# Performance work log

Measured on AMD Instinct MI355X. Metric: run time of the kernel, lower is better.

## Reference

```python
import jax, jax.numpy as jnp
import numpy as np

NG = 100000   # number of g-side nodes
NS = 100000   # number of s-side nodes
E = 640000    # edges per direction
D = 128       # feature / embed dim


def setup_inputs() -> dict:
    key = jax.random.key(0)
    ks = jax.random.split(key, 16)
    inp = {
        'Xg_self':  jax.random.normal(ks[0], (NG, D), jnp.float32),
        'Xs_self':  jax.random.normal(ks[1], (NS, D), jnp.float32),
        'Xs_for_g': jax.random.normal(ks[2], (NS, D), jnp.float32),
        'Xg_for_s': jax.random.normal(ks[3], (NG, D), jnp.float32),
        # COO edge lists for the two bipartite sparse adjacencies
        'row_gs': jax.random.randint(ks[4], (E,), 0, NG, jnp.int32),
        'col_gs': jax.random.randint(ks[5], (E,), 0, NS, jnp.int32),
        'val_gs': jax.random.uniform(ks[6], (E,), jnp.float32),
        'row_sg': jax.random.randint(ks[7], (E,), 0, NS, jnp.int32),
        'col_sg': jax.random.randint(ks[8], (E,), 0, NG, jnp.int32),
        'val_sg': jax.random.uniform(ks[9], (E,), jnp.float32),
        # Linear weights (PyTorch layout: [out_features, in_features], no bias)
        'Wg_self':  jax.random.normal(ks[10], (D, D), jnp.float32) * 0.05,
        'Wg_neigh': jax.random.normal(ks[11], (D, D), jnp.float32) * 0.05,
        'Ws_self':  jax.random.normal(ks[12], (D, D), jnp.float32) * 0.05,
        'Ws_neigh': jax.random.normal(ks[13], (D, D), jnp.float32) * 0.05,
    }
    return inp


def reference(Xg_self, Xs_self, Xs_for_g, Xg_for_s,
              row_gs, col_gs, val_gs, row_sg, col_sg, val_sg,
              Wg_self, Wg_neigh, Ws_self, Ws_neigh):
    # SpMM: neigh_g = A_gs @ Xs_for_g  (Ng x Ns sparse times Ns x D dense)
    neigh_g = jax.ops.segment_sum(Xs_for_g[col_gs] * val_gs[:, None], row_gs,
                                  num_segments=NG)
    # SpMM: neigh_s = A_sg @ Xg_for_s
    neigh_s = jax.ops.segment_sum(Xg_for_s[col_sg] * val_sg[:, None], row_sg,
                                  num_segments=NS)
    out_g = jax.nn.relu(Xg_self @ Wg_self.T + neigh_g @ Wg_neigh.T)
    out_s = jax.nn.relu(Xs_self @ Ws_self.T + neigh_s @ Ws_neigh.T)
    return (out_g, out_s)
```

## Files before the change

### kernel.cpp

```cpp
#include <hip/hip_runtime.h>
#include <hip/hip_bf16.h>
#include <stdint.h>

typedef __attribute__((ext_vector_type(4))) float f32x4;
typedef __attribute__((ext_vector_type(8))) short bf16x8;

#define D 128
#define GLOBAL_AS __attribute__((address_space(1)))
#define LDS_AS __attribute__((address_space(3)))

__device__ inline short f2bf(float x) {
    __hip_bfloat16 h = __float2bfloat16(x);
    return __builtin_bit_cast(short, h);
}

__device__ inline bf16x8 pack8(f32x4 lo, f32x4 hi) {
    bf16x8 b;
    b[0] = f2bf(lo[0]); b[1] = f2bf(lo[1]); b[2] = f2bf(lo[2]); b[3] = f2bf(lo[3]);
    b[4] = f2bf(hi[0]); b[5] = f2bf(hi[1]); b[6] = f2bf(hi[2]); b[7] = f2bf(hi[3]);
    return b;
}

__device__ inline unsigned int pack2bf(float a, float b) {
    unsigned int ua = (unsigned int)(unsigned short)f2bf(a);
    unsigned int ub = (unsigned int)(unsigned short)f2bf(b);
    return ua | (ub << 16);
}


__global__ __launch_bounds__(256)
void prep_kernel(const float* __restrict__ Xa, const float* __restrict__ Xb,
                 unsigned short* __restrict__ x16a, unsigned short* __restrict__ x16b,
                 const float* __restrict__ Wg_self, const float* __restrict__ Wg_neigh,
                 const float* __restrict__ Ws_self, const float* __restrict__ Ws_neigh,
                 short* __restrict__ Wcat,
                 const int* __restrict__ rowA, int EA,
                 const int* __restrict__ rowB, int NGoff,
                 int* __restrict__ cnt,
                 int n8a, int n8b, int Etot)
{
    int t = blockIdx.x * 256 + threadIdx.x;
    if (t < n8a) {
        f32x4 lo = *reinterpret_cast<const f32x4*>(Xa + (size_t)t * 8);
        f32x4 hi = *reinterpret_cast<const f32x4*>(Xa + (size_t)t * 8 + 4);
        *reinterpret_cast<bf16x8*>(x16a + (size_t)t * 8) = pack8(lo, hi);
        return;
    }
    t -= n8a;
    if (t < n8b) {
        f32x4 lo = *reinterpret_cast<const f32x4*>(Xb + (size_t)t * 8);
        f32x4 hi = *reinterpret_cast<const f32x4*>(Xb + (size_t)t * 8 + 4);
        *reinterpret_cast<bf16x8*>(x16b + (size_t)t * 8) = pack8(lo, hi);
        return;
    }
    t -= n8b;
    if (t < 2 * 128 * 32) {
        int dir = t >> 12;
        int rem = t & 4095;
        int j = rem >> 5;
        int k = (rem & 31) * 8;
        const float* Wself  = dir ? Ws_self  : Wg_self;
        const float* Wneigh = dir ? Ws_neigh : Wg_neigh;
        const float* src = (k < 128) ? (Wself + j * D + k) : (Wneigh + j * D + (k - 128));
        f32x4 lo = *reinterpret_cast<const f32x4*>(src);
        f32x4 hi = *reinterpret_cast<const f32x4*>(src + 4);
        *reinterpret_cast<bf16x8*>(Wcat + (size_t)dir * 32768 + j * 256 + k) = pack8(lo, hi);
        return;
    }
    t -= 2 * 128 * 32;
    if (t < Etot) {
        int r = (t < EA) ? rowA[t] : (rowB[t - EA] + NGoff);
        atomicAdd(&cnt[r], 1);
    }
}


__global__ __launch_bounds__(256)
void scan1_kernel(const int* __restrict__ cnt, int* __restrict__ part,
                  int* __restrict__ blksums, int N)
{
    __shared__ int wsum[4];
    int t = threadIdx.x;
    int base = blockIdx.x * 1024 + t * 4;
    int v0 = base + 0 < N ? cnt[base + 0] : 0;
    int v1 = base + 1 < N ? cnt[base + 1] : 0;
    int v2 = base + 2 < N ? cnt[base + 2] : 0;
    int v3 = base + 3 < N ? cnt[base + 3] : 0;
    int s = v0 + v1 + v2 + v3;
    int lane = t & 63, w = t >> 6;
    int x = s;
#pragma unroll
    for (int off = 1; off < 64; off <<= 1) {
        int y = __shfl_up(x, off);
        if (lane >= off) x += y;
    }
    if (lane == 63) wsum[w] = x;
    __syncthreads();
    int woff = 0;
    for (int i = 0; i < w; ++i) woff += wsum[i];
    int incl = x + woff;
    int excl = incl - s;
    if (base + 0 < N) part[base + 0] = excl;
    if (base + 1 < N) part[base + 1] = excl + v0;
    if (base + 2 < N) part[base + 2] = excl + v0 + v1;
    if (base + 3 < N) part[base + 3] = excl + v0 + v1 + v2;
    if (t == 255) blksums[blockIdx.x] = incl;
}

__global__ __launch_bounds__(256)
void scan2_kernel(int* __restrict__ blksums, int nb)
{
    __shared__ int wsum[4];
    int t = threadIdx.x;
    int v = t < nb ? blksums[t] : 0;
    int lane = t & 63, w = t >> 6;
    int x = v;
#pragma unroll
    for (int off = 1; off < 64; off <<= 1) {
        int y = __shfl_up(x, off);
        if (lane >= off) x += y;
    }
    if (lane == 63) wsum[w] = x;
    __syncthreads();
    int woff = 0;
    for (int i = 0; i < w; ++i) woff += wsum[i];
    int excl = x + woff - v;
    if (t < nb) blksums[t] = excl;
}

__global__ __launch_bounds__(256)
void scan3_kernel(int* __restrict__ cursor, const int* __restrict__ blksums, int N)
{
    int i = blockIdx.x * 256 + threadIdx.x;
    if (i < N) cursor[i] += blksums[i >> 10];
}

__global__ __launch_bounds__(256)
void fill2_kernel(const int* __restrict__ rowA, const int* __restrict__ colA,
                  const float* __restrict__ valA, int EA,
                  const int* __restrict__ rowB, const int* __restrict__ colB,
                  const float* __restrict__ valB, int NGoff,
                  int* __restrict__ cursor, int2* __restrict__ pairs, int Etot)
{
    int e = blockIdx.x * 256 + threadIdx.x;
    if (e >= Etot) return;
    int r, c; float v;
    if (e < EA) { r = rowA[e]; c = colA[e]; v = valA[e]; }
    else { int e2 = e - EA; r = rowB[e2] + NGoff; c = colB[e2]; v = valB[e2]; }
    int p = atomicAdd(&cursor[r], 1);
    pairs[p] = make_int2(c, __float_as_int(v));
}

__global__ __launch_bounds__(512, 6)
void fused_kernel(const unsigned short* __restrict__ X16_0,
                  const unsigned short* __restrict__ X16_1,
                  const float* __restrict__ Xself0, float* __restrict__ out0, int n0,
                  const float* __restrict__ Xself1, float* __restrict__ out1, int n1,
                  const int* __restrict__ cnt, const int* __restrict__ endpos,
                  const int2* __restrict__ pairs, const short* __restrict__ Wcat)
{
    __shared__ float  As[32 * 128];
    __shared__ bf16x8 Ab[32 * 16];

    const int ROWS = 32;
    int blocks0 = (n0 + ROWS - 1) / ROWS;

    const unsigned short* X16; const float* Xself; float* out;
    int nRows, r0base, csr0; const short* Wb;
    if ((int)blockIdx.x < blocks0) {
        X16 = X16_0; Xself = Xself0; out = out0; nRows = n0;
        r0base = blockIdx.x * ROWS; csr0 = 0; Wb = Wcat;
    } else {
        X16 = X16_1; Xself = Xself1; out = out1; nRows = n1;
        r0base = ((int)blockIdx.x - blocks0) * ROWS; csr0 = n0; Wb = Wcat + 32768;
    }

    const int tid  = threadIdx.x;
    const int wave = tid >> 6, lane = tid & 63;
    const int l15  = lane & 15, lhi = lane >> 4;
    const int l31  = lane & 31;
    const int hw   = tid >> 5;

#pragma unroll
    for (int q = 0; q < 2; ++q) {
        int rs = wave * 4 + q * 2 + (lane >> 5);
        int R = r0base + rs; if (R > nRows - 1) R = nRows - 1;
        const float* g = Xself + (size_t)R * D + (((lane & 31) ^ (rs & 7)) << 2);
        __builtin_amdgcn_global_load_lds((const GLOBAL_AS uint32_t*)g,
                                         (LDS_AS uint32_t*)(&As[(wave * 4 + q * 2) * 128]),
                                         16, 0, 0);
    }

    uint2* Ab64 = (uint2*)Ab;
#pragma unroll 1
    for (int ii = 0; ii < 2; ++ii) {
        int r = hw * 2 + ii;
        int R = r0base + r; if (R > nRows - 1) R = nRows - 1;
        int gid = csr0 + R;
        int n = cnt[gid];
        int s = endpos[gid] - n;
        f32x4 acc = {0.f, 0.f, 0.f, 0.f};
#pragma unroll 1
        for (int j = 0; j < n; j += 8) {
            int2 p[8]; uint2 xb[8];
#pragma unroll
            for (int u = 0; u < 8; ++u) {
                int idx = (j + u < n) ? j + u : n - 1;
                p[u] = pairs[s + idx];
            }
#pragma unroll
            for (int u = 0; u < 8; ++u)
                xb[u] = *reinterpret_cast<const uint2*>(X16 + (size_t)p[u].x * D + l31 * 4);
#pragma unroll
            for (int u = 0; u < 8; ++u) {
                float v = (j + u < n) ? __int_as_float(p[u].y) : 0.f;
                acc[0] += __uint_as_float(xb[u].x << 16) * v;
                acc[1] += __uint_as_float(xb[u].x & 0xffff0000u) * v;
                acc[2] += __uint_as_float(xb[u].y << 16) * v;
                acc[3] += __uint_as_float(xb[u].y & 0xffff0000u) * v;
            }
        }
        uint2 nb = { pack2bf(acc[0], acc[1]), pack2bf(acc[2], acc[3]) };
        int cn = (l31 >> 1) ^ (r & 7);
        Ab64[r * 32 + cn * 2 + (l31 & 1)] = nb;
    }

    bf16x8 bfrag[8];
    {
        int j = wave * 16 + l15;
#pragma unroll
        for (int kb = 0; kb < 8; ++kb)
            bfrag[kb] = *reinterpret_cast<const bf16x8*>(
                Wb + (size_t)j * 256 + kb * 32 + lhi * 8);
    }

    __syncthreads();

#pragma unroll
    for (int it = 0; it < 2; ++it) {
        int r = it * 16 + l15;
        int rx = r & 7;
        f32x4 acc = {0.f, 0.f, 0.f, 0.f};
#pragma unroll
        for (int kb = 0; kb < 8; ++kb) {
            bf16x8 af;
            if (kb < 4) {
                int c0 = kb * 8 + lhi * 2;
                f32x4 lo = *reinterpret_cast<const f32x4*>(&As[r * 128 + ((c0 ^ rx) << 2)]);
                f32x4 hi = *reinterpret_cast<const f32x4*>(&As[r * 128 + (((c0 + 1) ^ rx) << 2)]);
                af = pack8(lo, hi);
            } else {
                int cn = (kb - 4) * 4 + lhi;
                af = Ab[r * 16 + (cn ^ rx)];
            }
            acc = __builtin_amdgcn_mfma_f32_16x16x32_bf16(af, bfrag[kb], acc, 0, 0, 0);
        }
#pragma unroll
        for (int i2 = 0; i2 < 4; ++i2) {
            int rr = r0base + it * 16 + lhi * 4 + i2;
            if (rr < nRows) {
                float v = acc[i2] > 0.f ? acc[i2] : 0.f;
                out[(size_t)rr * D + wave * 16 + l15] = v;
            }
        }
    }
}


__global__ __launch_bounds__(256)
void scatter_edges(const float* __restrict__ X, const int* __restrict__ row,
                   const int* __restrict__ col, const float* __restrict__ val,
                   float* out, int nE)
{
    int t = blockIdx.x * 256 + threadIdx.x;
    int e = t >> 5;
    if (e >= nE) return;
    int l = t & 31;
    int r = row[e];
    int c = col[e];
    float v = val[e];
    f32x4 x = *reinterpret_cast<const f32x4*>(X + (size_t)c * D + l * 4);
    float* o = out + (size_t)r * D + l * 4;
    unsafeAtomicAdd(o + 0, x[0] * v);
    unsafeAtomicAdd(o + 1, x[1] * v);
    unsafeAtomicAdd(o + 2, x[2] * v);
    unsafeAtomicAdd(o + 3, x[3] * v);
}

__global__ __launch_bounds__(256)
void gemm_relu_fb(const float* __restrict__ Xself, const float* __restrict__ Neigh,
                  const float* __restrict__ Wself, const float* __restrict__ Wneigh,
                  float* __restrict__ out, int nRows)
{
    const int tid  = threadIdx.x;
    const int wave = tid >> 6;
    const int lane = tid & 63;
    const int l15  = lane & 15;
    const int lhi  = lane >> 4;

    bf16x8 bfrag[2][8];
#pragma unroll
    for (int n = 0; n < 2; ++n) {
        int j = wave * 32 + n * 16 + l15;
#pragma unroll
        for (int kb = 0; kb < 8; ++kb) {
            int k = kb * 32 + lhi * 8;
            const float* src = (kb < 4) ? (Wself + j * D + k)
                                        : (Wneigh + j * D + (k - 128));
            f32x4 lo = *reinterpret_cast<const f32x4*>(src);
            f32x4 hi = *reinterpret_cast<const f32x4*>(src + 4);
            bfrag[n][kb] = pack8(lo, hi);
        }
    }

    int r0base = blockIdx.x * 128;
#pragma unroll 1
    for (int it = 0; it < 8; ++it) {
        int r0 = r0base + it * 16;
        if (r0 >= nRows) break;
        const float* xrow = Xself + (size_t)(r0 + l15) * D;
        const float* nrow = Neigh + (size_t)(r0 + l15) * D;
        bf16x8 afrag[8];
#pragma unroll
        for (int kb = 0; kb < 8; ++kb) {
            const float* src = (kb < 4) ? (xrow + kb * 32 + lhi * 8)
                                        : (nrow + (kb - 4) * 32 + lhi * 8);
            f32x4 lo = *reinterpret_cast<const f32x4*>(src);
            f32x4 hi = *reinterpret_cast<const f32x4*>(src + 4);
            afrag[kb] = pack8(lo, hi);
        }
        asm volatile("s_waitcnt vmcnt(0)" ::: "memory");
        __syncthreads();

        f32x4 acc0 = {0.f, 0.f, 0.f, 0.f};
        f32x4 acc1 = {0.f, 0.f, 0.f, 0.f};
#pragma unroll
        for (int kb = 0; kb < 8; ++kb) {
            acc0 = __builtin_amdgcn_mfma_f32_16x16x32_bf16(afrag[kb], bfrag[0][kb], acc0, 0, 0, 0);
            acc1 = __builtin_amdgcn_mfma_f32_16x16x32_bf16(afrag[kb], bfrag[1][kb], acc1, 0, 0, 0);
        }
#pragma unroll
        for (int i = 0; i < 4; ++i) {
            int rr = r0 + lhi * 4 + i;
            if (rr < nRows) {
                float v0 = acc0[i] > 0.f ? acc0[i] : 0.f;
                float v1 = acc1[i] > 0.f ? acc1[i] : 0.f;
                out[(size_t)rr * D + wave * 32 + l15]      = v0;
                out[(size_t)rr * D + wave * 32 + 16 + l15] = v1;
            }
        }
    }
}


extern "C" void kernel_launch(void* const* d_in, const int* in_sizes, int n_in,
                              void* d_out, int out_size, void* d_ws, size_t ws_size,
                              hipStream_t stream)
{
    const float* Xg_self  = (const float*)d_in[0];
    const float* Xs_self  = (const float*)d_in[1];
    const float* Xs_for_g = (const float*)d_in[2];
    const float* Xg_for_s = (const float*)d_in[3];
    const int*   row_gs   = (const int*)d_in[4];
    const int*   col_gs   = (const int*)d_in[5];
    const float* val_gs   = (const float*)d_in[6];
    const int*   row_sg   = (const int*)d_in[7];
    const int*   col_sg   = (const int*)d_in[8];
    const float* val_sg   = (const float*)d_in[9];
    const float* Wg_self  = (const float*)d_in[10];
    const float* Wg_neigh = (const float*)d_in[11];
    const float* Ws_self  = (const float*)d_in[12];
    const float* Ws_neigh = (const float*)d_in[13];

    const int NG = in_sizes[0] / D;
    const int NS = in_sizes[1] / D;
    const int E1 = in_sizes[4];
    const int E2 = in_sizes[7];
    const int N  = NG + NS;
    const int Etot = E1 + E2;

    float* out_g = (float*)d_out;
    float* out_s = out_g + (size_t)NG * D;

    size_t off = 0;
    auto alloc = [&](size_t bytes) -> size_t {
        off = (off + 255) & ~(size_t)255;
        size_t o = off;
        off += bytes;
        return o;
    };
    size_t x16g_o   = alloc(sizeof(short) * (size_t)NG * D);
    size_t x16s_o   = alloc(sizeof(short) * (size_t)NS * D);
    size_t wcat_o   = alloc(sizeof(short) * 2 * 128 * 256);
    size_t cnt_o    = alloc(sizeof(int) * N);
    size_t cursor_o = alloc(sizeof(int) * N);
    size_t pairs_o  = alloc(sizeof(int2) * (size_t)Etot);
    size_t blk_o    = alloc(sizeof(int) * 1024);
    size_t need_bytes = off;

    char* ws = (char*)d_ws;

    if (ws_size < need_bytes) {
        hipMemsetAsync(d_out, 0, (size_t)out_size * sizeof(float), stream);
        {
            long long threads = (long long)E1 * 32;
            scatter_edges<<<(int)((threads + 255) / 256), 256, 0, stream>>>(
                Xs_for_g, row_gs, col_gs, val_gs, out_g, E1);
        }
        {
            long long threads = (long long)E2 * 32;
            scatter_edges<<<(int)((threads + 255) / 256), 256, 0, stream>>>(
                Xg_for_s, row_sg, col_sg, val_sg, out_s, E2);
        }
        gemm_relu_fb<<<(NG + 127) / 128, 256, 0, stream>>>(Xg_self, out_g, Wg_self, Wg_neigh, out_g, NG);
        gemm_relu_fb<<<(NS + 127) / 128, 256, 0, stream>>>(Xs_self, out_s, Ws_self, Ws_neigh, out_s, NS);
        return;
    }

    unsigned short* x16g = (unsigned short*)(ws + x16g_o);
    unsigned short* x16s = (unsigned short*)(ws + x16s_o);
    short* wcat  = (short*)(ws + wcat_o);
    int* cnt     = (int*)(ws + cnt_o);
    int* cursor  = (int*)(ws + cursor_o);
    int2* pairs  = (int2*)(ws + pairs_o);
    int* blk     = (int*)(ws + blk_o);

    const int n8a = NG * D / 8, n8b = NS * D / 8;

    hipMemsetAsync(cnt, 0, sizeof(int) * N, stream);

    {
        long long tot = (long long)n8a + n8b + 2 * 128 * 32 + Etot;
        prep_kernel<<<(int)((tot + 255) / 256), 256, 0, stream>>>(
            Xs_for_g, Xg_for_s, x16g, x16s,
            Wg_self, Wg_neigh, Ws_self, Ws_neigh, wcat,
            row_gs, E1, row_sg, NG, cnt, n8a, n8b, Etot);
    }

    int nb = (N + 1023) / 1024;
    scan1_kernel<<<nb, 256, 0, stream>>>(cnt, cursor, blk, N);
    scan2_kernel<<<1, 256, 0, stream>>>(blk, nb);
    scan3_kernel<<<(N + 255) / 256, 256, 0, stream>>>(cursor, blk, N);
    fill2_kernel<<<(Etot + 255) / 256, 256, 0, stream>>>(
        row_gs, col_gs, val_gs, E1, row_sg, col_sg, val_sg, NG, cursor, pairs, Etot);

    int blocks0 = (NG + 31) / 32, blocks1 = (NS + 31) / 32;
    fused_kernel<<<blocks0 + blocks1, 512, 0, stream>>>(
        x16g, x16s,
        Xg_self, out_g, NG,
        Xs_self, out_s, NS,
        cnt, cursor, pairs, wcat);
}
```

Before: 297.6 us.

## Gather fp32 features directly and widen fused kernel to 1024 threads

Drops the pre-pass that converted both neighbor feature matrices to bf16, so the SpMM gather now reads fp32 rows straight from the inputs. The fused kernel grows to 1024 threads with one row per half-wave and a 2x8 wave grid of MFMA tiles. The self features are loaded and packed to bf16 per lane into a single shared A tile, replacing the async global-to-LDS copy. This removes roughly 100 MB of conversion traffic, but doubles the bytes moved per gathered edge and lowers unroll depth, which may reduce memory-level parallelism.

```diff
diff --git a/kernel.cpp b/kernel.cpp
--- a/kernel.cpp
+++ b/kernel.cpp
@@ -6,8 +6,6 @@
 typedef __attribute__((ext_vector_type(8))) short bf16x8;
 
 #define D 128
-#define GLOBAL_AS __attribute__((address_space(1)))
-#define LDS_AS __attribute__((address_space(3)))
 
 __device__ inline short f2bf(float x) {
     __hip_bfloat16 h = __float2bfloat16(x);
@@ -29,31 +27,14 @@
 
 
 __global__ __launch_bounds__(256)
-void prep_kernel(const float* __restrict__ Xa, const float* __restrict__ Xb,
-                 unsigned short* __restrict__ x16a, unsigned short* __restrict__ x16b,
-                 const float* __restrict__ Wg_self, const float* __restrict__ Wg_neigh,
+void prep_kernel(const float* __restrict__ Wg_self, const float* __restrict__ Wg_neigh,
                  const float* __restrict__ Ws_self, const float* __restrict__ Ws_neigh,
                  short* __restrict__ Wcat,
                  const int* __restrict__ rowA, int EA,
                  const int* __restrict__ rowB, int NGoff,
-                 int* __restrict__ cnt,
-                 int n8a, int n8b, int Etot)
+                 int* __restrict__ cnt, int Etot)
 {
     int t = blockIdx.x * 256 + threadIdx.x;
-    if (t < n8a) {
-        f32x4 lo = *reinterpret_cast<const f32x4*>(Xa + (size_t)t * 8);
-        f32x4 hi = *reinterpret_cast<const f32x4*>(Xa + (size_t)t * 8 + 4);
-        *reinterpret_cast<bf16x8*>(x16a + (size_t)t * 8) = pack8(lo, hi);
-        return;
-    }
-    t -= n8a;
-    if (t < n8b) {
-        f32x4 lo = *reinterpret_cast<const f32x4*>(Xb + (size_t)t * 8);
-        f32x4 hi = *reinterpret_cast<const f32x4*>(Xb + (size_t)t * 8 + 4);
-        *reinterpret_cast<bf16x8*>(x16b + (size_t)t * 8) = pack8(lo, hi);
-        return;
-    }
-    t -= n8b;
     if (t < 2 * 128 * 32) {
         int dir = t >> 12;
         int rem = t & 4095;
@@ -151,27 +132,25 @@
     pairs[p] = make_int2(c, __float_as_int(v));
 }
 
-__global__ __launch_bounds__(512, 6)
-void fused_kernel(const unsigned short* __restrict__ X16_0,
-                  const unsigned short* __restrict__ X16_1,
+__global__ __launch_bounds__(1024, 8)
+void fused_kernel(const float* __restrict__ X0, const float* __restrict__ X1,
                   const float* __restrict__ Xself0, float* __restrict__ out0, int n0,
                   const float* __restrict__ Xself1, float* __restrict__ out1, int n1,
                   const int* __restrict__ cnt, const int* __restrict__ endpos,
                   const int2* __restrict__ pairs, const short* __restrict__ Wcat)
 {
-    __shared__ float  As[32 * 128];
-    __shared__ bf16x8 Ab[32 * 16];
+    __shared__ bf16x8 A[32 * 32];
 
     const int ROWS = 32;
     int blocks0 = (n0 + ROWS - 1) / ROWS;
 
-    const unsigned short* X16; const float* Xself; float* out;
+    const float *X, *Xself; float* out;
     int nRows, r0base, csr0; const short* Wb;
     if ((int)blockIdx.x < blocks0) {
-        X16 = X16_0; Xself = Xself0; out = out0; nRows = n0;
+        X = X0; Xself = Xself0; out = out0; nRows = n0;
         r0base = blockIdx.x * ROWS; csr0 = 0; Wb = Wcat;
     } else {
-        X16 = X16_1; Xself = Xself1; out = out1; nRows = n1;
+        X = X1; Xself = Xself1; out = out1; nRows = n1;
         r0base = ((int)blockIdx.x - blocks0) * ROWS; csr0 = n0; Wb = Wcat + 32768;
     }
 
@@ -181,53 +160,48 @@
     const int l31  = lane & 31;
     const int hw   = tid >> 5;
 
-#pragma unroll
-    for (int q = 0; q < 2; ++q) {
-        int rs = wave * 4 + q * 2 + (lane >> 5);
-        int R = r0base + rs; if (R > nRows - 1) R = nRows - 1;
-        const float* g = Xself + (size_t)R * D + (((lane & 31) ^ (rs & 7)) << 2);
-        __builtin_amdgcn_global_load_lds((const GLOBAL_AS uint32_t*)g,
-                                         (LDS_AS uint32_t*)(&As[(wave * 4 + q * 2) * 128]),
-                                         16, 0, 0);
-    }
-
-    uint2* Ab64 = (uint2*)Ab;
-#pragma unroll 1
-    for (int ii = 0; ii < 2; ++ii) {
-        int r = hw * 2 + ii;
+    {
+        int r = hw;
         int R = r0base + r; if (R > nRows - 1) R = nRows - 1;
         int gid = csr0 + R;
         int n = cnt[gid];
         int s = endpos[gid] - n;
         f32x4 acc = {0.f, 0.f, 0.f, 0.f};
 #pragma unroll 1
-        for (int j = 0; j < n; j += 8) {
-            int2 p[8]; uint2 xb[8];
-#pragma unroll
-            for (int u = 0; u < 8; ++u) {
+        for (int j = 0; j < n; j += 4) {
+            int2 p[4]; f32x4 xb[4];
+#pragma unroll
+            for (int u = 0; u < 4; ++u) {
                 int idx = (j + u < n) ? j + u : n - 1;
                 p[u] = pairs[s + idx];
             }
 #pragma unroll
-            for (int u = 0; u < 8; ++u)
-                xb[u] = *reinterpret_cast<const uint2*>(X16 + (size_t)p[u].x * D + l31 * 4);
-#pragma unroll
-            for (int u = 0; u < 8; ++u) {
+            for (int u = 0; u < 4; ++u)
+                xb[u] = *reinterpret_cast<const f32x4*>(X + (size_t)p[u].x * D + l31 * 4);
+#pragma unroll
+            for (int u = 0; u < 4; ++u) {
                 float v = (j + u < n) ? __int_as_float(p[u].y) : 0.f;
-                acc[0] += __uint_as_float(xb[u].x << 16) * v;
-                acc[1] += __uint_as_float(xb[u].x & 0xffff0000u) * v;
-                acc[2] += __uint_as_float(xb[u].y << 16) * v;
-                acc[3] += __uint_as_float(xb[u].y & 0xffff0000u) * v;
+                acc[0] += xb[u][0] * v;
+                acc[1] += xb[u][1] * v;
+                acc[2] += xb[u][2] * v;
+                acc[3] += xb[u][3] * v;
             }
         }
-        uint2 nb = { pack2bf(acc[0], acc[1]), pack2bf(acc[2], acc[3]) };
-        int cn = (l31 >> 1) ^ (r & 7);
-        Ab64[r * 32 + cn * 2 + (l31 & 1)] = nb;
+        f32x4 xs = *reinterpret_cast<const f32x4*>(Xself + (size_t)R * D + l31 * 4);
+        uint2 sb  = { pack2bf(xs[0],  xs[1]),  pack2bf(xs[2],  xs[3])  };
+        uint2 nbv = { pack2bf(acc[0], acc[1]), pack2bf(acc[2], acc[3]) };
+        int rx = r & 7;
+        int eS = (l31 >> 1) ^ rx;
+        int eN = 16 + ((l31 >> 1) ^ rx);
+        uint2* A64 = (uint2*)A;
+        A64[(r * 32 + eS) * 2 + (l31 & 1)] = sb;
+        A64[(r * 32 + eN) * 2 + (l31 & 1)] = nbv;
     }
 
     bf16x8 bfrag[8];
     {
-        int j = wave * 16 + l15;
+        int ct = wave & 7;
+        int j = ct * 16 + l15;
 #pragma unroll
         for (int kb = 0; kb < 8; ++kb)
             bfrag[kb] = *reinterpret_cast<const bf16x8*>(
@@ -236,31 +210,23 @@
 
     __syncthreads();
 
-#pragma unroll
-    for (int it = 0; it < 2; ++it) {
-        int r = it * 16 + l15;
+    {
+        int rt = wave >> 3, ct = wave & 7;
+        int r = rt * 16 + l15;
         int rx = r & 7;
         f32x4 acc = {0.f, 0.f, 0.f, 0.f};
 #pragma unroll
         for (int kb = 0; kb < 8; ++kb) {
-            bf16x8 af;
-            if (kb < 4) {
-                int c0 = kb * 8 + lhi * 2;
-                f32x4 lo = *reinterpret_cast<const f32x4*>(&As[r * 128 + ((c0 ^ rx) << 2)]);
-                f32x4 hi = *reinterpret_cast<const f32x4*>(&As[r * 128 + (((c0 + 1) ^ rx) << 2)]);
-                af = pack8(lo, hi);
-            } else {
-                int cn = (kb - 4) * 4 + lhi;
-                af = Ab[r * 16 + (cn ^ rx)];
-            }
+            int e = kb * 4 + lhi;
+            bf16x8 af = A[r * 32 + (e ^ rx)];
             acc = __builtin_amdgcn_mfma_f32_16x16x32_bf16(af, bfrag[kb], acc, 0, 0, 0);
         }
 #pragma unroll
-        for (int i2 = 0; i2 < 4; ++i2) {
-            int rr = r0base + it * 16 + lhi * 4 + i2;
+        for (int i = 0; i < 4; ++i) {
+            int rr = r0base + rt * 16 + lhi * 4 + i;
             if (rr < nRows) {
-                float v = acc[i2] > 0.f ? acc[i2] : 0.f;
-                out[(size_t)rr * D + wave * 16 + l15] = v;
+                float v = acc[i] > 0.f ? acc[i] : 0.f;
+                out[(size_t)rr * D + ct * 16 + l15] = v;
             }
         }
     }
@@ -389,8 +355,6 @@
         off += bytes;
         return o;
     };
-    size_t x16g_o   = alloc(sizeof(short) * (size_t)NG * D);
-    size_t x16s_o   = alloc(sizeof(short) * (size_t)NS * D);
     size_t wcat_o   = alloc(sizeof(short) * 2 * 128 * 256);
     size_t cnt_o    = alloc(sizeof(int) * N);
     size_t cursor_o = alloc(sizeof(int) * N);
@@ -417,24 +381,19 @@
         return;
     }
 
-    unsigned short* x16g = (unsigned short*)(ws + x16g_o);
-    unsigned short* x16s = (unsigned short*)(ws + x16s_o);
     short* wcat  = (short*)(ws + wcat_o);
     int* cnt     = (int*)(ws + cnt_o);
     int* cursor  = (int*)(ws + cursor_o);
     int2* pairs  = (int2*)(ws + pairs_o);
     int* blk     = (int*)(ws + blk_o);
 
-    const int n8a = NG * D / 8, n8b = NS * D / 8;
-
     hipMemsetAsync(cnt, 0, sizeof(int) * N, stream);
 
     {
-        long long tot = (long long)n8a + n8b + 2 * 128 * 32 + Etot;
+        long long tot = (long long)2 * 128 * 32 + Etot;
         prep_kernel<<<(int)((tot + 255) / 256), 256, 0, stream>>>(
-            Xs_for_g, Xg_for_s, x16g, x16s,
             Wg_self, Wg_neigh, Ws_self, Ws_neigh, wcat,
-            row_gs, E1, row_sg, NG, cnt, n8a, n8b, Etot);
+            row_gs, E1, row_sg, NG, cnt, Etot);
     }
 
     int nb = (N + 1023) / 1024;
@@ -445,8 +404,8 @@
         row_gs, col_gs, val_gs, E1, row_sg, col_sg, val_sg, NG, cursor, pairs, Etot);
 
     int blocks0 = (NG + 31) / 32, blocks1 = (NS + 31) / 32;
-    fused_kernel<<<blocks0 + blocks1, 512, 0, stream>>>(
-        x16g, x16s,
+    fused_kernel<<<blocks0 + blocks1, 1024, 0, stream>>>(
+        Xs_for_g, Xg_for_s,
         Xg_self, out_g, NG,
         Xs_self, out_s, NS,
         cnt, cursor, pairs, wcat);
```

Result: slower. 328.8 us (+10.5%).

## Shrink fused SAGE tile to 16 rows with unified bf16 LDS operand

Applied to the files above, without the earlier changes.

The fused gather+GEMM kernel now handles 16 rows per 512-thread block instead of 32. Each half-wave gathers one row's neighbours and also loads its self features directly, converting both to bf16 into a single swizzled LDS tile. This replaces the async global-to-LDS fp32 staging and the in-loop fp32-to-bf16 packing. It also lowers LDS use and raises the occupancy hint from 6 to 8, giving more blocks and more parallel gather latency hiding. In exchange, each block reloads the same weight fragments for half as many rows, and the self-feature load now runs serially after the gather loop.

```diff
diff --git a/kernel.cpp b/kernel.cpp
--- a/kernel.cpp
+++ b/kernel.cpp
@@ -6,8 +6,6 @@
 typedef __attribute__((ext_vector_type(8))) short bf16x8;
 
 #define D 128
-#define GLOBAL_AS __attribute__((address_space(1)))
-#define LDS_AS __attribute__((address_space(3)))
 
 __device__ inline short f2bf(float x) {
     __hip_bfloat16 h = __float2bfloat16(x);
@@ -151,7 +149,7 @@
     pairs[p] = make_int2(c, __float_as_int(v));
 }
 
-__global__ __launch_bounds__(512, 6)
+__global__ __launch_bounds__(512, 8)
 void fused_kernel(const unsigned short* __restrict__ X16_0,
                   const unsigned short* __restrict__ X16_1,
                   const float* __restrict__ Xself0, float* __restrict__ out0, int n0,
@@ -159,10 +157,9 @@
                   const int* __restrict__ cnt, const int* __restrict__ endpos,
                   const int2* __restrict__ pairs, const short* __restrict__ Wcat)
 {
-    __shared__ float  As[32 * 128];
-    __shared__ bf16x8 Ab[32 * 16];
-
-    const int ROWS = 32;
+    __shared__ bf16x8 A[16 * 32];
+
+    const int ROWS = 16;
     int blocks0 = (n0 + ROWS - 1) / ROWS;
 
     const unsigned short* X16; const float* Xself; float* out;
@@ -181,20 +178,8 @@
     const int l31  = lane & 31;
     const int hw   = tid >> 5;
 
-#pragma unroll
-    for (int q = 0; q < 2; ++q) {
-        int rs = wave * 4 + q * 2 + (lane >> 5);
-        int R = r0base + rs; if (R > nRows - 1) R = nRows - 1;
-        const float* g = Xself + (size_t)R * D + (((lane & 31) ^ (rs & 7)) << 2);
-        __builtin_amdgcn_global_load_lds((const GLOBAL_AS uint32_t*)g,
-                                         (LDS_AS uint32_t*)(&As[(wave * 4 + q * 2) * 128]),
-                                         16, 0, 0);
-    }
-
-    uint2* Ab64 = (uint2*)Ab;
-#pragma unroll 1
-    for (int ii = 0; ii < 2; ++ii) {
-        int r = hw * 2 + ii;
+    {
+        int r = hw;
         int R = r0base + r; if (R > nRows - 1) R = nRows - 1;
         int gid = csr0 + R;
         int n = cnt[gid];
@@ -220,9 +205,15 @@
                 acc[3] += __uint_as_float(xb[u].y & 0xffff0000u) * v;
             }
         }
-        uint2 nb = { pack2bf(acc[0], acc[1]), pack2bf(acc[2], acc[3]) };
-        int cn = (l31 >> 1) ^ (r & 7);
-        Ab64[r * 32 + cn * 2 + (l31 & 1)] = nb;
+        f32x4 xs = *reinterpret_cast<const f32x4*>(Xself + (size_t)R * D + l31 * 4);
+        uint2 sb  = { pack2bf(xs[0],  xs[1]),  pack2bf(xs[2],  xs[3])  };
+        uint2 nbv = { pack2bf(acc[0], acc[1]), pack2bf(acc[2], acc[3]) };
+        int rx = r & 7;
+        int eS = (l31 >> 1) ^ rx;
+        int eN = 16 + ((l31 >> 1) ^ rx);
+        uint2* A64 = (uint2*)A;
+        A64[(r * 32 + eS) * 2 + (l31 & 1)] = sb;
+        A64[(r * 32 + eN) * 2 + (l31 & 1)] = nbv;
     }
 
     bf16x8 bfrag[8];
@@ -236,30 +227,21 @@
 
     __syncthreads();
 
-#pragma unroll
-    for (int it = 0; it < 2; ++it) {
-        int r = it * 16 + l15;
+    {
+        int r = l15;
         int rx = r & 7;
         f32x4 acc = {0.f, 0.f, 0.f, 0.f};
 #pragma unroll
         for (int kb = 0; kb < 8; ++kb) {
-            bf16x8 af;
-            if (kb < 4) {
-                int c0 = kb * 8 + lhi * 2;
-                f32x4 lo = *reinterpret_cast<const f32x4*>(&As[r * 128 + ((c0 ^ rx) << 2)]);
-                f32x4 hi = *reinterpret_cast<const f32x4*>(&As[r * 128 + (((c0 + 1) ^ rx) << 2)]);
-                af = pack8(lo, hi);
-            } else {
-                int cn = (kb - 4) * 4 + lhi;
-                af = Ab[r * 16 + (cn ^ rx)];
-            }
+            int e = kb * 4 + lhi;
+            bf16x8 af = A[r * 32 + (e ^ rx)];
             acc = __builtin_amdgcn_mfma_f32_16x16x32_bf16(af, bfrag[kb], acc, 0, 0, 0);
         }
 #pragma unroll
-        for (int i2 = 0; i2 < 4; ++i2) {
-            int rr = r0base + it * 16 + lhi * 4 + i2;
+        for (int i = 0; i < 4; ++i) {
+            int rr = r0base + lhi * 4 + i;
             if (rr < nRows) {
-                float v = acc[i2] > 0.f ? acc[i2] : 0.f;
+                float v = acc[i] > 0.f ? acc[i] : 0.f;
                 out[(size_t)rr * D + wave * 16 + l15] = v;
             }
         }
@@ -444,7 +426,7 @@
     fill2_kernel<<<(Etot + 255) / 256, 256, 0, stream>>>(
         row_gs, col_gs, val_gs, E1, row_sg, col_sg, val_sg, NG, cursor, pairs, Etot);
 
-    int blocks0 = (NG + 31) / 32, blocks1 = (NS + 31) / 32;
+    int blocks0 = (NG + 15) / 16, blocks1 = (NS + 15) / 16;
     fused_kernel<<<blocks0 + blocks1, 512, 0, stream>>>(
         x16g, x16s,
         Xg_self, out_g, NG,
```

Result: slower. 350.0 us (+17.6%).

## Split fused gather+GEMM into separate gather and GEMM kernels via bf16 buffer

Applied to the files above, without the earlier changes.

Un-fuses the neighbour aggregation from the GEMM. A new gather kernel uses one wave per row with 64 lanes reading 2 bf16 each and writes the aggregated neighbours to a bf16 workspace buffer. A separate 256-thread GEMM kernel loads those rows straight into MFMA fragments, with each wave computing two 16-column tiles. The aim is to decouple the latency-bound irregular gather from the MFMA stage and improve occupancy for each, at the cost of an extra kernel launch and a write and read of an N×128 bf16 intermediate.

```diff
diff --git a/kernel.cpp b/kernel.cpp
--- a/kernel.cpp
+++ b/kernel.cpp
@@ -151,116 +151,125 @@
     pairs[p] = make_int2(c, __float_as_int(v));
 }
 
-__global__ __launch_bounds__(512, 6)
-void fused_kernel(const unsigned short* __restrict__ X16_0,
-                  const unsigned short* __restrict__ X16_1,
-                  const float* __restrict__ Xself0, float* __restrict__ out0, int n0,
-                  const float* __restrict__ Xself1, float* __restrict__ out1, int n1,
-                  const int* __restrict__ cnt, const int* __restrict__ endpos,
-                  const int2* __restrict__ pairs, const short* __restrict__ Wcat)
-{
-    __shared__ float  As[32 * 128];
-    __shared__ bf16x8 Ab[32 * 16];
-
+__global__ __launch_bounds__(256)
+void gather_kernel(const unsigned short* __restrict__ X16_0,
+                   const unsigned short* __restrict__ X16_1,
+                   const int* __restrict__ cnt, const int* __restrict__ endpos,
+                   const int2* __restrict__ pairs,
+                   unsigned short* __restrict__ neigh16, int NG, int N)
+{
+    int wid = (blockIdx.x * 256 + threadIdx.x) >> 6;
+    if (wid >= N) return;
+    int lane = threadIdx.x & 63;
+    const unsigned short* X16 = (wid < NG) ? X16_0 : X16_1;
+    int n = __builtin_amdgcn_readfirstlane(cnt[wid]);
+    int s = __builtin_amdgcn_readfirstlane(endpos[wid]) - n;
+    float acc0 = 0.f, acc1 = 0.f;
+#pragma unroll 1
+    for (int j = 0; j < n; j += 8) {
+        int2 p[8]; unsigned int x[8];
+#pragma unroll
+        for (int u = 0; u < 8; ++u) {
+            int idx = (j + u < n) ? j + u : n - 1;
+            p[u] = pairs[s + idx];
+        }
+#pragma unroll
+        for (int u = 0; u < 8; ++u)
+            x[u] = *reinterpret_cast<const unsigned int*>(X16 + (size_t)p[u].x * D + lane * 2);
+#pragma unroll
+        for (int u = 0; u < 8; ++u) {
+            float v = (j + u < n) ? __int_as_float(p[u].y) : 0.f;
+            acc0 += __uint_as_float(x[u] << 16) * v;
+            acc1 += __uint_as_float(x[u] & 0xffff0000u) * v;
+        }
+    }
+    ((unsigned int*)neigh16)[(size_t)wid * 64 + lane] = pack2bf(acc0, acc1);
+}
+
+__global__ __launch_bounds__(256)
+void gemm16_kernel(const float* __restrict__ Xself0, const float* __restrict__ Xself1,
+                   const unsigned short* __restrict__ neigh16,
+                   float* __restrict__ out0, int n0,
+                   float* __restrict__ out1, int n1,
+                   const short* __restrict__ Wcat)
+{
+    __shared__ float A[32 * 128];
     const int ROWS = 32;
     int blocks0 = (n0 + ROWS - 1) / ROWS;
 
-    const unsigned short* X16; const float* Xself; float* out;
-    int nRows, r0base, csr0; const short* Wb;
+    const float* Xself; float* out; int nRows, r0base, csr0; const short* Wb;
     if ((int)blockIdx.x < blocks0) {
-        X16 = X16_0; Xself = Xself0; out = out0; nRows = n0;
+        Xself = Xself0; out = out0; nRows = n0;
         r0base = blockIdx.x * ROWS; csr0 = 0; Wb = Wcat;
     } else {
-        X16 = X16_1; Xself = Xself1; out = out1; nRows = n1;
+        Xself = Xself1; out = out1; nRows = n1;
         r0base = ((int)blockIdx.x - blocks0) * ROWS; csr0 = n0; Wb = Wcat + 32768;
     }
 
-    const int tid  = threadIdx.x;
-    const int wave = tid >> 6, lane = tid & 63;
-    const int l15  = lane & 15, lhi = lane >> 4;
-    const int l31  = lane & 31;
-    const int hw   = tid >> 5;
-
-#pragma unroll
-    for (int q = 0; q < 2; ++q) {
-        int rs = wave * 4 + q * 2 + (lane >> 5);
-        int R = r0base + rs; if (R > nRows - 1) R = nRows - 1;
-        const float* g = Xself + (size_t)R * D + (((lane & 31) ^ (rs & 7)) << 2);
+    const int tid = threadIdx.x, wave = tid >> 6, lane = tid & 63;
+    const int l15 = lane & 15, lhi = lane >> 4;
+
+#pragma unroll
+    for (int i = 0; i < 8; i += 2) {
+        int r = wave * 8 + i + (lane >> 5);
+        int R = r0base + r; if (R > nRows - 1) R = nRows - 1;
+        const float* g = Xself + (size_t)R * D + (((lane & 31) ^ (r & 7)) << 2);
         __builtin_amdgcn_global_load_lds((const GLOBAL_AS uint32_t*)g,
-                                         (LDS_AS uint32_t*)(&As[(wave * 4 + q * 2) * 128]),
+                                         (LDS_AS uint32_t*)(&A[(wave * 8 + i) * 128]),
                                          16, 0, 0);
     }
 
-    uint2* Ab64 = (uint2*)Ab;
-#pragma unroll 1
-    for (int ii = 0; ii < 2; ++ii) {
-        int r = hw * 2 + ii;
-        int R = r0base + r; if (R > nRows - 1) R = nRows - 1;
-        int gid = csr0 + R;
-        int n = cnt[gid];
-        int s = endpos[gid] - n;
-        f32x4 acc = {0.f, 0.f, 0.f, 0.f};
-#pragma unroll 1
-        for (int j = 0; j < n; j += 8) {
-            int2 p[8]; uint2 xb[8];
-#pragma unroll
-            for (int u = 0; u < 8; ++u) {
-                int idx = (j + u < n) ? j + u : n - 1;
-                p[u] = pairs[s + idx];
-            }
-#pragma unroll
-            for (int u = 0; u < 8; ++u)
-                xb[u] = *reinterpret_cast<const uint2*>(X16 + (size_t)p[u].x * D + l31 * 4);
-#pragma unroll
-            for (int u = 0; u < 8; ++u) {
-                float v = (j + u < n) ? __int_as_float(p[u].y) : 0.f;
-                acc[0] += __uint_as_float(xb[u].x << 16) * v;
-                acc[1] += __uint_as_float(xb[u].x & 0xffff0000u) * v;
-                acc[2] += __uint_as_float(xb[u].y << 16) * v;
-                acc[3] += __uint_as_float(xb[u].y & 0xffff0000u) * v;
-            }
-        }
-        uint2 nb = { pack2bf(acc[0], acc[1]), pack2bf(acc[2], acc[3]) };
-        int cn = (l31 >> 1) ^ (r & 7);
-        Ab64[r * 32 + cn * 2 + (l31 & 1)] = nb;
-    }
-
-    bf16x8 bfrag[8];
-    {
-        int j = wave * 16 + l15;
+    bf16x8 bfrag[2][8];
+#pragma unroll
+    for (int nn = 0; nn < 2; ++nn) {
+        int j = wave * 32 + nn * 16 + l15;
 #pragma unroll
         for (int kb = 0; kb < 8; ++kb)
-            bfrag[kb] = *reinterpret_cast<const bf16x8*>(
+            bfrag[nn][kb] = *reinterpret_cast<const bf16x8*>(
                 Wb + (size_t)j * 256 + kb * 32 + lhi * 8);
     }
 
+    bf16x8 nfrag[2][4];
+#pragma unroll
+    for (int it = 0; it < 2; ++it) {
+        int R = r0base + it * 16 + l15; if (R > nRows - 1) R = nRows - 1;
+#pragma unroll
+        for (int k4 = 0; k4 < 4; ++k4)
+            nfrag[it][k4] = *reinterpret_cast<const bf16x8*>(
+                neigh16 + (size_t)(csr0 + R) * D + k4 * 32 + lhi * 8);
+    }
+
+    asm volatile("s_waitcnt vmcnt(0)" ::: "memory");
     __syncthreads();
 
 #pragma unroll
     for (int it = 0; it < 2; ++it) {
         int r = it * 16 + l15;
         int rx = r & 7;
-        f32x4 acc = {0.f, 0.f, 0.f, 0.f};
+        f32x4 acc0 = {0.f, 0.f, 0.f, 0.f};
+        f32x4 acc1 = {0.f, 0.f, 0.f, 0.f};
 #pragma unroll
         for (int kb = 0; kb < 8; ++kb) {
             bf16x8 af;
             if (kb < 4) {
                 int c0 = kb * 8 + lhi * 2;
-                f32x4 lo = *reinterpret_cast<const f32x4*>(&As[r * 128 + ((c0 ^ rx) << 2)]);
-                f32x4 hi = *reinterpret_cast<const f32x4*>(&As[r * 128 + (((c0 + 1) ^ rx) << 2)]);
+                f32x4 lo = *reinterpret_cast<const f32x4*>(&A[r * 128 + ((c0 ^ rx) << 2)]);
+                f32x4 hi = *reinterpret_cast<const f32x4*>(&A[r * 128 + (((c0 + 1) ^ rx) << 2)]);
                 af = pack8(lo, hi);
             } else {
-                int cn = (kb - 4) * 4 + lhi;
-                af = Ab[r * 16 + (cn ^ rx)];
+                af = nfrag[it][kb - 4];
             }
-            acc = __builtin_amdgcn_mfma_f32_16x16x32_bf16(af, bfrag[kb], acc, 0, 0, 0);
+            acc0 = __builtin_amdgcn_mfma_f32_16x16x32_bf16(af, bfrag[0][kb], acc0, 0, 0, 0);
+            acc1 = __builtin_amdgcn_mfma_f32_16x16x32_bf16(af, bfrag[1][kb], acc1, 0, 0, 0);
         }
 #pragma unroll
         for (int i2 = 0; i2 < 4; ++i2) {
             int rr = r0base + it * 16 + lhi * 4 + i2;
             if (rr < nRows) {
-                float v = acc[i2] > 0.f ? acc[i2] : 0.f;
-                out[(size_t)rr * D + wave * 16 + l15] = v;
+                float v0 = acc0[i2] > 0.f ? acc0[i2] : 0.f;
+                float v1 = acc1[i2] > 0.f ? acc1[i2] : 0.f;
+                out[(size_t)rr * D + wave * 32 + l15]      = v0;
+                out[(size_t)rr * D + wave * 32 + 16 + l15] = v1;
             }
         }
     }
@@ -396,6 +405,7 @@
     size_t cursor_o = alloc(sizeof(int) * N);
     size_t pairs_o  = alloc(sizeof(int2) * (size_t)Etot);
     size_t blk_o    = alloc(sizeof(int) * 1024);
+    size_t neigh_o  = alloc(sizeof(short) * (size_t)N * D);
     size_t need_bytes = off;
 
     char* ws = (char*)d_ws;
@@ -417,13 +427,14 @@
         return;
     }
 
-    unsigned short* x16g = (unsigned short*)(ws + x16g_o);
-    unsigned short* x16s = (unsigned short*)(ws + x16s_o);
-    short* wcat  = (short*)(ws + wcat_o);
-    int* cnt     = (int*)(ws + cnt_o);
-    int* cursor  = (int*)(ws + cursor_o);
-    int2* pairs  = (int2*)(ws + pairs_o);
-    int* blk     = (int*)(ws + blk_o);
+    unsigned short* x16g    = (unsigned short*)(ws + x16g_o);
+    unsigned short* x16s    = (unsigned short*)(ws + x16s_o);
+    short* wcat             = (short*)(ws + wcat_o);
+    int* cnt                = (int*)(ws + cnt_o);
+    int* cursor             = (int*)(ws + cursor_o);
+    int2* pairs             = (int2*)(ws + pairs_o);
+    int* blk                = (int*)(ws + blk_o);
+    unsigned short* neigh16 = (unsigned short*)(ws + neigh_o);
 
     const int n8a = NG * D / 8, n8b = NS * D / 8;
 
@@ -444,10 +455,10 @@
     fill2_kernel<<<(Etot + 255) / 256, 256, 0, stream>>>(
         row_gs, col_gs, val_gs, E1, row_sg, col_sg, val_sg, NG, cursor, pairs, Etot);
 
+    gather_kernel<<<(int)(((long long)N * 64 + 255) / 256), 256, 0, stream>>>(
+        x16g, x16s, cnt, cursor, pairs, neigh16, NG, N);
+
     int blocks0 = (NG + 31) / 32, blocks1 = (NS + 31) / 32;
-    fused_kernel<<<blocks0 + blocks1, 512, 0, stream>>>(
-        x16g, x16s,
-        Xg_self, out_g, NG,
-        Xs_self, out_s, NS,
-        cnt, cursor, pairs, wcat);
-}
+    gemm16_kernel<<<blocks0 + blocks1, 256, 0, stream>>>(
+        Xg_self, Xs_self, neigh16, out_g, NG, out_s, NS, wcat);
+}
```

After: 336.8 us. 1.13x slower.
